# Performance work log

Measured on AMD Instinct MI355X. Metric: run time of the kernel, lower is better.

Reference implementation:

```python
import jax, jax.numpy as jnp
import numpy as np

HEADS = 4
DIM_HEAD = 32
SCALE = DIM_HEAD ** -0.5


def setup_inputs() -> dict:
    key = jax.random.key(0)
    k1, k2, k3 = jax.random.split(key, 3)
    dim = 128
    hidden = HEADS * DIM_HEAD  # 128
    x = jax.random.normal(k1, (4, dim, 64, 64), dtype=jnp.float32)
    w_qkv = jax.random.normal(k2, (3 * hidden, dim), dtype=jnp.float32) * (dim ** -0.5)
    w_out = jax.random.normal(k3, (dim, hidden), dtype=jnp.float32) * (hidden ** -0.5)
    b_out = jnp.zeros((dim,), dtype=jnp.float32)
    return {"x": x, "w_qkv": w_qkv, "w_out": w_out, "b_out": b_out}


def reference(x, w_qkv, w_out, b_out):
    b, c, h, w = x.shape
    n = h * w
    # 1x1 conv == channel matmul per pixel
    qkv = jnp.einsum('oc,bchw->bohw', w_qkv, x)  # [b, 3*hidden, h, w]
    q, k, v = jnp.split(qkv, 3, axis=1)
    # b (heads d) x y -> b heads d (x y)
    def to_heads(t):
        return t.reshape(b, HEADS, DIM_HEAD, n)
    q = to_heads(q) * SCALE
    k = to_heads(k)
    v = to_heads(v)
    sim = jnp.einsum('bhdi,bhdj->bhij', q, k)          # [b, heads, n, n]
    attn = jax.nn.softmax(sim, axis=-1)
    out = jnp.einsum('bhij,bhdj->bhid', attn, v)        # [b, heads, n, d]
    # b h (x y) d -> b (h d) x y
    out = out.transpose(0, 1, 3, 2).reshape(b, HEADS * DIM_HEAD, h, w)
    out = jnp.einsum('oc,bchw->bohw', w_out, out) + b_out[None, :, None, None]
    return out
```

## Files before the change

### kernel.cpp

```cpp
#include <hip/hip_runtime.h>
#include <math.h>

#define NHEAD 4
#define DHEAD 32
#define NPIX  4096
#define CIN   128

typedef __bf16 bf16_t;
typedef __bf16 bf16x8 __attribute__((ext_vector_type(8)));
typedef __bf16 bf16x4 __attribute__((ext_vector_type(4)));
typedef float  f32x4  __attribute__((ext_vector_type(4)));

constexpr float QSCALE = 0.17677669529663687f * 1.4426950408889634f;

__global__ void __launch_bounds__(256) prep_weights(
    const float* __restrict__ w_qkv, const float* __restrict__ w_out,
    ushort* __restrict__ wqkv_bf, ushort* __restrict__ wout_bf) {
  const int i4 = (blockIdx.x * 256 + threadIdx.x) * 4;
  const float* src;
  ushort* dst;
  float sc = 1.f;
  if (i4 < 49152) {
    src = w_qkv + i4; dst = wqkv_bf + i4;
    if (i4 < 16384) sc = QSCALE;
  } else {
    src = w_out + (i4 - 49152); dst = wout_bf + (i4 - 49152);
  }
  float4 v = *(const float4*)src;
  bf16x4 o = {(bf16_t)(v.x * sc), (bf16_t)(v.y * sc),
              (bf16_t)(v.z * sc), (bf16_t)(v.w * sc)};
  *(bf16x4*)dst = o;
}

__global__ void __launch_bounds__(384) qkv_mfma(
    const float* __restrict__ x, const ushort* __restrict__ wqkv,
    ushort* __restrict__ qb, ushort* __restrict__ kb, ushort* __restrict__ vT) {
  __shared__ ushort Xls[32 * 136];
  const int tid = threadIdx.x, cg = tid >> 6, lane = tid & 63;
  const int n = lane & 15, quad = lane >> 4;
  const int b = blockIdx.y, p0 = blockIdx.x * 32;

  bf16x8 wf[4][4];
#pragma unroll
  for (int t1 = 0; t1 < 4; ++t1)
#pragma unroll
    for (int k = 0; k < 4; ++k)
      wf[t1][k] = *(const bf16x8*)(wqkv +
          (size_t)(cg * 64 + t1 * 16 + n) * CIN + k * 32 + quad * 8);

  if (tid < 256) {
    const int pc = tid & 7;
    const int c  = (tid >> 3) * 4;
    const float* xp = x + ((size_t)b * CIN + c) * NPIX + p0 + pc * 4;
    float4 r0 = *(const float4*)xp;
    float4 r1 = *(const float4*)(xp + NPIX);
    float4 r2 = *(const float4*)(xp + 2 * NPIX);
    float4 r3 = *(const float4*)(xp + 3 * NPIX);
    bf16x4 w0 = {(bf16_t)r0.x, (bf16_t)r1.x, (bf16_t)r2.x, (bf16_t)r3.x};
    bf16x4 w1 = {(bf16_t)r0.y, (bf16_t)r1.y, (bf16_t)r2.y, (bf16_t)r3.y};
    bf16x4 w2 = {(bf16_t)r0.z, (bf16_t)r1.z, (bf16_t)r2.z, (bf16_t)r3.z};
    bf16x4 w3 = {(bf16_t)r0.w, (bf16_t)r1.w, (bf16_t)r2.w, (bf16_t)r3.w};
    *(bf16x4*)&Xls[(pc * 4 + 0) * 136 + c] = w0;
    *(bf16x4*)&Xls[(pc * 4 + 1) * 136 + c] = w1;
    *(bf16x4*)&Xls[(pc * 4 + 2) * 136 + c] = w2;
    *(bf16x4*)&Xls[(pc * 4 + 3) * 136 + c] = w3;
  }
  __syncthreads();

  f32x4 acc[4][2];
#pragma unroll
  for (int i = 0; i < 4; ++i)
#pragma unroll
    for (int j = 0; j < 2; ++j) acc[i][j] = (f32x4){0.f, 0.f, 0.f, 0.f};

  const bool isv = (cg >= 4);
#pragma unroll
  for (int k = 0; k < 4; ++k) {
    bf16x8 xf[2];
#pragma unroll
    for (int pt = 0; pt < 2; ++pt)
      xf[pt] = *(const bf16x8*)&Xls[(pt * 16 + n) * 136 + k * 32 + quad * 8];
    if (!isv) {
#pragma unroll
      for (int wt = 0; wt < 4; ++wt)
#pragma unroll
        for (int pt = 0; pt < 2; ++pt)
          acc[wt][pt] = __builtin_amdgcn_mfma_f32_16x16x32_bf16(
              wf[wt][k], xf[pt], acc[wt][pt], 0, 0, 0);
    } else {
#pragma unroll
      for (int ct = 0; ct < 4; ++ct)
#pragma unroll
        for (int pt = 0; pt < 2; ++pt)
          acc[ct][pt] = __builtin_amdgcn_mfma_f32_16x16x32_bf16(
              xf[pt], wf[ct][k], acc[ct][pt], 0, 0, 0);
    }
  }

  if (!isv) {
    ushort* dst0 = (cg < 2) ? qb : kb;
#pragma unroll
    for (int wt = 0; wt < 4; ++wt) {
      const int ch = (cg & 1) * 64 + wt * 16 + quad * 4;
      const int head = ch >> 5, d = ch & 31;
#pragma unroll
      for (int pt = 0; pt < 2; ++pt) {
        const int p = p0 + pt * 16 + n;
        f32x4 a = acc[wt][pt];
        bf16x4 o = {(bf16_t)a[0], (bf16_t)a[1], (bf16_t)a[2], (bf16_t)a[3]};
        *(bf16x4*)(dst0 + ((size_t)(b * NHEAD + head) * NPIX + p) * DHEAD + d) = o;
      }
    }
  } else {
#pragma unroll
    for (int ct = 0; ct < 4; ++ct) {
      const int ch = (cg & 1) * 64 + ct * 16 + n;
      const int head = ch >> 5, d = ch & 31;
#pragma unroll
      for (int pt = 0; pt < 2; ++pt) {
        const int p = p0 + pt * 16 + quad * 4;
        f32x4 a = acc[ct][pt];
        bf16x4 o = {(bf16_t)a[0], (bf16_t)a[1], (bf16_t)a[2], (bf16_t)a[3]};
        *(bf16x4*)(vT + ((size_t)(b * NHEAD + head) * DHEAD + d) * NPIX + p) = o;
      }
    }
  }
}

__device__ __forceinline__ void ft_load(const ushort* kb0, const ushort* vb0,
                                        int t, bf16x8* kf, bf16x8* vf) {
#pragma unroll
  for (int p = 0; p < 2; ++p) {
#pragma unroll
    for (int s = 0; s < 2; ++s)
      kf[p * 2 + s] = *(const bf16x8*)(kb0 + (size_t)(t * 64 + p * 32 + s * 4) * DHEAD);
#pragma unroll
    for (int dp = 0; dp < 2; ++dp)
      vf[p * 2 + dp] = *(const bf16x8*)(vb0 + (size_t)dp * 16 * NPIX + t * 64 + p * 32);
  }
}

__device__ __forceinline__ void ft_compute(const bf16x8* qf, const bf16x8* kf,
                                           const bf16x8* vf, const bf16x8 ones,
                                           f32x4 O[8][2], f32x4* Ol) {
  const f32x4 zero = {0.f, 0.f, 0.f, 0.f};
#pragma unroll
  for (int p = 0; p < 2; ++p) {
#pragma unroll
    for (int rp = 0; rp < 8; ++rp) {
      f32x4 sa = __builtin_amdgcn_mfma_f32_16x16x32_bf16(kf[p * 2 + 0], qf[rp], zero, 0, 0, 0);
      f32x4 sb = __builtin_amdgcn_mfma_f32_16x16x32_bf16(kf[p * 2 + 1], qf[rp], zero, 0, 0, 0);
      bf16x8 pf;
#pragma unroll
      for (int r = 0; r < 4; ++r) {
        pf[r]     = (bf16_t)__builtin_amdgcn_exp2f(sa[r]);
        pf[r + 4] = (bf16_t)__builtin_amdgcn_exp2f(sb[r]);
      }
      O[rp][0] = __builtin_amdgcn_mfma_f32_16x16x32_bf16(pf, vf[p * 2 + 0], O[rp][0], 0, 0, 0);
      O[rp][1] = __builtin_amdgcn_mfma_f32_16x16x32_bf16(pf, vf[p * 2 + 1], O[rp][1], 0, 0, 0);
      Ol[rp]   = __builtin_amdgcn_mfma_f32_16x16x32_bf16(pf, ones, Ol[rp], 0, 0, 0);
    }
  }
}

__global__ void __launch_bounds__(256, 2) flash_mfma(
    const ushort* __restrict__ qb, const ushort* __restrict__ kbuf,
    const ushort* __restrict__ vTb, float* __restrict__ part) {
  const int tid = threadIdx.x, wave = tid >> 6, lane = tid & 63;
  const int n = lane & 15, quad = lane >> 4;
  const int js = blockIdx.y, bh = blockIdx.z;
  const int qrel = blockIdx.x * 512 + wave * 128;

  const ushort* kg = kbuf + (size_t)bh * NPIX * DHEAD;
  const ushort* vg = vTb + (size_t)bh * DHEAD * NPIX;

  bf16x8 qf[8];
#pragma unroll
  for (int rp = 0; rp < 8; ++rp)
    qf[rp] = *(const bf16x8*)(qb +
        ((size_t)bh * NPIX + qrel + rp * 16 + n) * DHEAD + quad * 8);

  f32x4 O[8][2], Ol[8];
#pragma unroll
  for (int rp = 0; rp < 8; ++rp) {
    O[rp][0] = (f32x4){0.f, 0.f, 0.f, 0.f};
    O[rp][1] = (f32x4){0.f, 0.f, 0.f, 0.f};
    Ol[rp]   = (f32x4){0.f, 0.f, 0.f, 0.f};
  }
  const bf16_t one = (bf16_t)1.0f;
  const bf16x8 ones = {one, one, one, one, one, one, one, one};

  const int pk = ((n >> 2) << 3) | (n & 3);
  const ushort* kb0 = kg + (size_t)(js * 1024 + pk) * DHEAD + quad * 8;
  const ushort* vb0 = vg + (size_t)n * NPIX + js * 1024 + quad * 8;

  bf16x8 kA[4], vA[4], kB[4], vB[4];
  ft_load(kb0, vb0, 0, kA, vA);
#pragma unroll 1
  for (int t = 0; t < 16; t += 2) {
    ft_load(kb0, vb0, t + 1, kB, vB);
    ft_compute(qf, kA, vA, ones, O, Ol);
    if (t + 2 < 16) ft_load(kb0, vb0, t + 2, kA, vA);
    ft_compute(qf, kB, vB, ones, O, Ol);
  }

  float* pb = part + ((size_t)js * 65536 + (size_t)bh * NPIX + qrel) * 36;
#pragma unroll
  for (int rp = 0; rp < 8; ++rp)
#pragma unroll
    for (int r = 0; r < 4; ++r) {
      const int q = rp * 16 + quad * 4 + r;
      pb[(size_t)q * 36 + n]      = O[rp][0][r];
      pb[(size_t)q * 36 + 16 + n] = O[rp][1][r];
      if (n == 0) pb[(size_t)q * 36 + 32] = Ol[rp][r];
    }
}

__global__ void __launch_bounds__(256) combine4(
    const float* __restrict__ part, ushort* __restrict__ aoT) {
  const int idx = blockIdx.x * 256 + threadIdx.x;
  const float* p0 = part + (size_t)idx * 36;
  const float* p1 = p0 + (size_t)65536 * 36;
  const float* p2 = p1 + (size_t)65536 * 36;
  const float* p3 = p2 + (size_t)65536 * 36;
  const float inv = 1.f / (p0[32] + p1[32] + p2[32] + p3[32]);
#pragma unroll
  for (int t = 0; t < 4; ++t) {
    float4 a0 = ((const float4*)p0)[2 * t], a1 = ((const float4*)p0)[2 * t + 1];
    float4 b0 = ((const float4*)p1)[2 * t], b1 = ((const float4*)p1)[2 * t + 1];
    float4 c0 = ((const float4*)p2)[2 * t], c1 = ((const float4*)p2)[2 * t + 1];
    float4 d0 = ((const float4*)p3)[2 * t], d1 = ((const float4*)p3)[2 * t + 1];
    bf16x8 o = {(bf16_t)((a0.x + b0.x + c0.x + d0.x) * inv),
                (bf16_t)((a0.y + b0.y + c0.y + d0.y) * inv),
                (bf16_t)((a0.z + b0.z + c0.z + d0.z) * inv),
                (bf16_t)((a0.w + b0.w + c0.w + d0.w) * inv),
                (bf16_t)((a1.x + b1.x + c1.x + d1.x) * inv),
                (bf16_t)((a1.y + b1.y + c1.y + d1.y) * inv),
                (bf16_t)((a1.z + b1.z + c1.z + d1.z) * inv),
                (bf16_t)((a1.w + b1.w + c1.w + d1.w) * inv)};
    *(bf16x8*)(aoT + (size_t)idx * 32 + t * 8) = o;
  }
}

__global__ void __launch_bounds__(512) out_mfma(
    const ushort* __restrict__ aoT, const ushort* __restrict__ wob,
    const float* __restrict__ bias, float* __restrict__ out) {
  const int tid = threadIdx.x, wv = tid >> 6, lane = tid & 63;
  const int n = lane & 15, quad = lane >> 4;
  const int b = blockIdx.y;
  const int oc0 = (wv & 1) * 64;
  const int p = blockIdx.x * 64 + (wv >> 1) * 16 + n;

  bf16x8 wf[4][4];
#pragma unroll
  for (int mt = 0; mt < 4; ++mt)
#pragma unroll
    for (int k = 0; k < 4; ++k)
      wf[mt][k] = *(const bf16x8*)(wob + (size_t)(oc0 + mt * 16 + n) * CIN + k * 32 + quad * 8);

  bf16x8 bfr[4];
#pragma unroll
  for (int k = 0; k < 4; ++k)
    bfr[k] = *(const bf16x8*)(aoT + ((size_t)(b * NHEAD + k) * NPIX + p) * DHEAD + quad * 8);

  f32x4 acc[4];
#pragma unroll
  for (int mt = 0; mt < 4; ++mt) acc[mt] = (f32x4){0.f, 0.f, 0.f, 0.f};
#pragma unroll
  for (int k = 0; k < 4; ++k)
#pragma unroll
    for (int mt = 0; mt < 4; ++mt)
      acc[mt] = __builtin_amdgcn_mfma_f32_16x16x32_bf16(wf[mt][k], bfr[k], acc[mt], 0, 0, 0);

#pragma unroll
  for (int mt = 0; mt < 4; ++mt) {
    const int oc = oc0 + mt * 16 + quad * 4;
#pragma unroll
    for (int r = 0; r < 4; ++r)
      out[((size_t)b * CIN + oc + r) * NPIX + p] = acc[mt][r] + bias[oc + r];
  }
}

extern "C" void kernel_launch(void* const* d_in, const int* in_sizes, int n_in,
                              void* d_out, int out_size, void* d_ws, size_t ws_size,
                              hipStream_t stream) {
  const float* x     = (const float*)d_in[0];
  const float* w_qkv = (const float*)d_in[1];
  const float* w_out = (const float*)d_in[2];
  const float* b_out = (const float*)d_in[3];
  float* out = (float*)d_out;

  char* base = (char*)d_ws;
  ushort* qb      = (ushort*)base;
  ushort* kb      = (ushort*)(base + (size_t)4 * 1024 * 1024);
  ushort* vT      = (ushort*)(base + (size_t)8 * 1024 * 1024);
  ushort* aoT     = (ushort*)(base + (size_t)12 * 1024 * 1024);
  ushort* wqkv_bf = (ushort*)(base + (size_t)16 * 1024 * 1024);
  ushort* wout_bf = (ushort*)(base + (size_t)16 * 1024 * 1024 + 96 * 1024);
  float*  part    = (float*)(base + (size_t)17 * 1024 * 1024);

  prep_weights<<<dim3(64), 256, 0, stream>>>(w_qkv, w_out, wqkv_bf, wout_bf);
  qkv_mfma<<<dim3(128, 4), 384, 0, stream>>>(x, wqkv_bf, qb, kb, vT);
  flash_mfma<<<dim3(8, 4, 16), 256, 0, stream>>>(qb, kb, vT, part);
  combine4<<<dim3(256), 256, 0, stream>>>(part, aoT);
  out_mfma<<<dim3(64, 4), 512, 0, stream>>>(aoT, wout_bf, b_out, out);
}
```

Baseline: 140.4 us.

## Fuse split-KV combine into flash kernel and fold weight casts into GEMMs

The flash kernel now splits the keys across the four waves of a block instead of across grid blocks. Each wave holds 64 query rows and processes a 1024-key slice, and the partial sums are reduced through shared memory inside the kernel, so the separate combine kernel and its global partial buffer go away. The weight prep kernel is removed; the QKV and output GEMM kernels read fp32 weights and convert them (with the Q scale) in registers. This cuts two launches and a large global round trip, but each wave now does a smaller tile with less Q reuse, and the weights are converted redundantly in every block.

```diff
diff --git a/kernel.cpp b/kernel.cpp
--- a/kernel.cpp
+++ b/kernel.cpp
@@ -13,40 +13,28 @@
 
 constexpr float QSCALE = 0.17677669529663687f * 1.4426950408889634f;
 
-__global__ void __launch_bounds__(256) prep_weights(
-    const float* __restrict__ w_qkv, const float* __restrict__ w_out,
-    ushort* __restrict__ wqkv_bf, ushort* __restrict__ wout_bf) {
-  const int i4 = (blockIdx.x * 256 + threadIdx.x) * 4;
-  const float* src;
-  ushort* dst;
-  float sc = 1.f;
-  if (i4 < 49152) {
-    src = w_qkv + i4; dst = wqkv_bf + i4;
-    if (i4 < 16384) sc = QSCALE;
-  } else {
-    src = w_out + (i4 - 49152); dst = wout_bf + (i4 - 49152);
-  }
-  float4 v = *(const float4*)src;
-  bf16x4 o = {(bf16_t)(v.x * sc), (bf16_t)(v.y * sc),
-              (bf16_t)(v.z * sc), (bf16_t)(v.w * sc)};
-  *(bf16x4*)dst = o;
-}
-
 __global__ void __launch_bounds__(384) qkv_mfma(
-    const float* __restrict__ x, const ushort* __restrict__ wqkv,
+    const float* __restrict__ x, const float* __restrict__ wqkv,
     ushort* __restrict__ qb, ushort* __restrict__ kb, ushort* __restrict__ vT) {
   __shared__ ushort Xls[32 * 136];
   const int tid = threadIdx.x, cg = tid >> 6, lane = tid & 63;
   const int n = lane & 15, quad = lane >> 4;
   const int b = blockIdx.y, p0 = blockIdx.x * 32;
 
+  const float wsc = (cg < 2) ? QSCALE : 1.0f;
   bf16x8 wf[4][4];
 #pragma unroll
   for (int t1 = 0; t1 < 4; ++t1)
 #pragma unroll
-    for (int k = 0; k < 4; ++k)
-      wf[t1][k] = *(const bf16x8*)(wqkv +
-          (size_t)(cg * 64 + t1 * 16 + n) * CIN + k * 32 + quad * 8);
+    for (int k = 0; k < 4; ++k) {
+      const float* wp = wqkv + (size_t)(cg * 64 + t1 * 16 + n) * CIN + k * 32 + quad * 8;
+      float4 a = *(const float4*)wp;
+      float4 c = *(const float4*)(wp + 4);
+      wf[t1][k] = (bf16x8){(bf16_t)(a.x * wsc), (bf16_t)(a.y * wsc),
+                           (bf16_t)(a.z * wsc), (bf16_t)(a.w * wsc),
+                           (bf16_t)(c.x * wsc), (bf16_t)(c.y * wsc),
+                           (bf16_t)(c.z * wsc), (bf16_t)(c.w * wsc)};
+    }
 
   if (tid < 256) {
     const int pc = tid & 7;
@@ -127,62 +115,55 @@
   }
 }
 
-__device__ __forceinline__ void ft_load(const ushort* kb0, const ushort* vb0,
-                                        int t, bf16x8* kf, bf16x8* vf) {
-#pragma unroll
-  for (int p = 0; p < 2; ++p) {
-#pragma unroll
-    for (int s = 0; s < 2; ++s)
-      kf[p * 2 + s] = *(const bf16x8*)(kb0 + (size_t)(t * 64 + p * 32 + s * 4) * DHEAD);
-#pragma unroll
-    for (int dp = 0; dp < 2; ++dp)
-      vf[p * 2 + dp] = *(const bf16x8*)(vb0 + (size_t)dp * 16 * NPIX + t * 64 + p * 32);
-  }
-}
-
-__device__ __forceinline__ void ft_compute(const bf16x8* qf, const bf16x8* kf,
-                                           const bf16x8* vf, const bf16x8 ones,
-                                           f32x4 O[8][2], f32x4* Ol) {
+__device__ __forceinline__ void fl_load(const ushort* kb0, const ushort* vb0,
+                                        int st, bf16x8* f) {
+  f[0] = *(const bf16x8*)(kb0 + (size_t)(st * 32) * DHEAD);
+  f[1] = *(const bf16x8*)(kb0 + (size_t)(st * 32 + 4) * DHEAD);
+  f[2] = *(const bf16x8*)(vb0 + st * 32);
+  f[3] = *(const bf16x8*)(vb0 + (size_t)16 * NPIX + st * 32);
+}
+
+__device__ __forceinline__ void fl_compute(const bf16x8* qf, const bf16x8* f,
+                                           const bf16x8 ones,
+                                           f32x4 O[4][2], f32x4* Ol) {
   const f32x4 zero = {0.f, 0.f, 0.f, 0.f};
 #pragma unroll
-  for (int p = 0; p < 2; ++p) {
-#pragma unroll
-    for (int rp = 0; rp < 8; ++rp) {
-      f32x4 sa = __builtin_amdgcn_mfma_f32_16x16x32_bf16(kf[p * 2 + 0], qf[rp], zero, 0, 0, 0);
-      f32x4 sb = __builtin_amdgcn_mfma_f32_16x16x32_bf16(kf[p * 2 + 1], qf[rp], zero, 0, 0, 0);
-      bf16x8 pf;
-#pragma unroll
-      for (int r = 0; r < 4; ++r) {
-        pf[r]     = (bf16_t)__builtin_amdgcn_exp2f(sa[r]);
-        pf[r + 4] = (bf16_t)__builtin_amdgcn_exp2f(sb[r]);
-      }
-      O[rp][0] = __builtin_amdgcn_mfma_f32_16x16x32_bf16(pf, vf[p * 2 + 0], O[rp][0], 0, 0, 0);
-      O[rp][1] = __builtin_amdgcn_mfma_f32_16x16x32_bf16(pf, vf[p * 2 + 1], O[rp][1], 0, 0, 0);
-      Ol[rp]   = __builtin_amdgcn_mfma_f32_16x16x32_bf16(pf, ones, Ol[rp], 0, 0, 0);
-    }
-  }
-}
-
-__global__ void __launch_bounds__(256, 2) flash_mfma(
+  for (int rp = 0; rp < 4; ++rp) {
+    f32x4 sa = __builtin_amdgcn_mfma_f32_16x16x32_bf16(f[0], qf[rp], zero, 0, 0, 0);
+    f32x4 sb = __builtin_amdgcn_mfma_f32_16x16x32_bf16(f[1], qf[rp], zero, 0, 0, 0);
+    bf16x8 pf;
+#pragma unroll
+    for (int r = 0; r < 4; ++r) {
+      pf[r]     = (bf16_t)__builtin_amdgcn_exp2f(sa[r]);
+      pf[r + 4] = (bf16_t)__builtin_amdgcn_exp2f(sb[r]);
+    }
+    O[rp][0] = __builtin_amdgcn_mfma_f32_16x16x32_bf16(pf, f[2], O[rp][0], 0, 0, 0);
+    O[rp][1] = __builtin_amdgcn_mfma_f32_16x16x32_bf16(pf, f[3], O[rp][1], 0, 0, 0);
+    Ol[rp]   = __builtin_amdgcn_mfma_f32_16x16x32_bf16(pf, ones, Ol[rp], 0, 0, 0);
+  }
+}
+
+__global__ void __launch_bounds__(256, 4) flash_mfma(
     const ushort* __restrict__ qb, const ushort* __restrict__ kbuf,
-    const ushort* __restrict__ vTb, float* __restrict__ part) {
+    const ushort* __restrict__ vTb, ushort* __restrict__ aoT) {
+  __shared__ float Ols[4][64][34];
   const int tid = threadIdx.x, wave = tid >> 6, lane = tid & 63;
   const int n = lane & 15, quad = lane >> 4;
-  const int js = blockIdx.y, bh = blockIdx.z;
-  const int qrel = blockIdx.x * 512 + wave * 128;
+  const int bh = blockIdx.y;
+  const int q0 = blockIdx.x * 64;
 
   const ushort* kg = kbuf + (size_t)bh * NPIX * DHEAD;
   const ushort* vg = vTb + (size_t)bh * DHEAD * NPIX;
 
-  bf16x8 qf[8];
-#pragma unroll
-  for (int rp = 0; rp < 8; ++rp)
+  bf16x8 qf[4];
+#pragma unroll
+  for (int rp = 0; rp < 4; ++rp)
     qf[rp] = *(const bf16x8*)(qb +
-        ((size_t)bh * NPIX + qrel + rp * 16 + n) * DHEAD + quad * 8);
-
-  f32x4 O[8][2], Ol[8];
-#pragma unroll
-  for (int rp = 0; rp < 8; ++rp) {
+        ((size_t)bh * NPIX + q0 + rp * 16 + n) * DHEAD + quad * 8);
+
+  f32x4 O[4][2], Ol[4];
+#pragma unroll
+  for (int rp = 0; rp < 4; ++rp) {
     O[rp][0] = (f32x4){0.f, 0.f, 0.f, 0.f};
     O[rp][1] = (f32x4){0.f, 0.f, 0.f, 0.f};
     Ol[rp]   = (f32x4){0.f, 0.f, 0.f, 0.f};
@@ -191,59 +172,46 @@
   const bf16x8 ones = {one, one, one, one, one, one, one, one};
 
   const int pk = ((n >> 2) << 3) | (n & 3);
-  const ushort* kb0 = kg + (size_t)(js * 1024 + pk) * DHEAD + quad * 8;
-  const ushort* vb0 = vg + (size_t)n * NPIX + js * 1024 + quad * 8;
-
-  bf16x8 kA[4], vA[4], kB[4], vB[4];
-  ft_load(kb0, vb0, 0, kA, vA);
+  const ushort* kb0 = kg + (size_t)(wave * 1024 + pk) * DHEAD + quad * 8;
+  const ushort* vb0 = vg + (size_t)n * NPIX + wave * 1024 + quad * 8;
+
+  bf16x8 fA[4], fB[4];
+  fl_load(kb0, vb0, 0, fA);
 #pragma unroll 1
-  for (int t = 0; t < 16; t += 2) {
-    ft_load(kb0, vb0, t + 1, kB, vB);
-    ft_compute(qf, kA, vA, ones, O, Ol);
-    if (t + 2 < 16) ft_load(kb0, vb0, t + 2, kA, vA);
-    ft_compute(qf, kB, vB, ones, O, Ol);
-  }
-
-  float* pb = part + ((size_t)js * 65536 + (size_t)bh * NPIX + qrel) * 36;
-#pragma unroll
-  for (int rp = 0; rp < 8; ++rp)
+  for (int st = 0; st < 32; st += 2) {
+    fl_load(kb0, vb0, st + 1, fB);
+    fl_compute(qf, fA, ones, O, Ol);
+    if (st + 2 < 32) fl_load(kb0, vb0, st + 2, fA);
+    fl_compute(qf, fB, ones, O, Ol);
+  }
+
+  float* W = &Ols[wave][0][0];
+#pragma unroll
+  for (int rp = 0; rp < 4; ++rp)
 #pragma unroll
     for (int r = 0; r < 4; ++r) {
       const int q = rp * 16 + quad * 4 + r;
-      pb[(size_t)q * 36 + n]      = O[rp][0][r];
-      pb[(size_t)q * 36 + 16 + n] = O[rp][1][r];
-      if (n == 0) pb[(size_t)q * 36 + 32] = Ol[rp][r];
-    }
-}
-
-__global__ void __launch_bounds__(256) combine4(
-    const float* __restrict__ part, ushort* __restrict__ aoT) {
-  const int idx = blockIdx.x * 256 + threadIdx.x;
-  const float* p0 = part + (size_t)idx * 36;
-  const float* p1 = p0 + (size_t)65536 * 36;
-  const float* p2 = p1 + (size_t)65536 * 36;
-  const float* p3 = p2 + (size_t)65536 * 36;
-  const float inv = 1.f / (p0[32] + p1[32] + p2[32] + p3[32]);
-#pragma unroll
-  for (int t = 0; t < 4; ++t) {
-    float4 a0 = ((const float4*)p0)[2 * t], a1 = ((const float4*)p0)[2 * t + 1];
-    float4 b0 = ((const float4*)p1)[2 * t], b1 = ((const float4*)p1)[2 * t + 1];
-    float4 c0 = ((const float4*)p2)[2 * t], c1 = ((const float4*)p2)[2 * t + 1];
-    float4 d0 = ((const float4*)p3)[2 * t], d1 = ((const float4*)p3)[2 * t + 1];
-    bf16x8 o = {(bf16_t)((a0.x + b0.x + c0.x + d0.x) * inv),
-                (bf16_t)((a0.y + b0.y + c0.y + d0.y) * inv),
-                (bf16_t)((a0.z + b0.z + c0.z + d0.z) * inv),
-                (bf16_t)((a0.w + b0.w + c0.w + d0.w) * inv),
-                (bf16_t)((a1.x + b1.x + c1.x + d1.x) * inv),
-                (bf16_t)((a1.y + b1.y + c1.y + d1.y) * inv),
-                (bf16_t)((a1.z + b1.z + c1.z + d1.z) * inv),
-                (bf16_t)((a1.w + b1.w + c1.w + d1.w) * inv)};
-    *(bf16x8*)(aoT + (size_t)idx * 32 + t * 8) = o;
-  }
+      W[q * 34 + n]      = O[rp][0][r];
+      W[q * 34 + 16 + n] = O[rp][1][r];
+      if (n == 0) W[q * 34 + 32] = Ol[rp][r];
+    }
+  __syncthreads();
+
+  const int q = tid >> 2, dg = tid & 3;
+  const float l = Ols[0][q][32] + Ols[1][q][32] + Ols[2][q][32] + Ols[3][q][32];
+  const float inv = 1.f / l;
+  bf16x8 o8;
+#pragma unroll
+  for (int e = 0; e < 8; ++e) {
+    const int d = dg * 8 + e;
+    const float s = Ols[0][q][d] + Ols[1][q][d] + Ols[2][q][d] + Ols[3][q][d];
+    o8[e] = (bf16_t)(s * inv);
+  }
+  *(bf16x8*)(aoT + ((size_t)bh * NPIX + q0 + q) * DHEAD + dg * 8) = o8;
 }
 
 __global__ void __launch_bounds__(512) out_mfma(
-    const ushort* __restrict__ aoT, const ushort* __restrict__ wob,
+    const ushort* __restrict__ aoT, const float* __restrict__ wout,
     const float* __restrict__ bias, float* __restrict__ out) {
   const int tid = threadIdx.x, wv = tid >> 6, lane = tid & 63;
   const int n = lane & 15, quad = lane >> 4;
@@ -255,8 +223,13 @@
 #pragma unroll
   for (int mt = 0; mt < 4; ++mt)
 #pragma unroll
-    for (int k = 0; k < 4; ++k)
-      wf[mt][k] = *(const bf16x8*)(wob + (size_t)(oc0 + mt * 16 + n) * CIN + k * 32 + quad * 8);
+    for (int k = 0; k < 4; ++k) {
+      const float* wp = wout + (size_t)(oc0 + mt * 16 + n) * CIN + k * 32 + quad * 8;
+      float4 a = *(const float4*)wp;
+      float4 c = *(const float4*)(wp + 4);
+      wf[mt][k] = (bf16x8){(bf16_t)a.x, (bf16_t)a.y, (bf16_t)a.z, (bf16_t)a.w,
+                           (bf16_t)c.x, (bf16_t)c.y, (bf16_t)c.z, (bf16_t)c.w};
+    }
 
   bf16x8 bfr[4];
 #pragma unroll
@@ -291,17 +264,12 @@
   float* out = (float*)d_out;
 
   char* base = (char*)d_ws;
-  ushort* qb      = (ushort*)base;
-  ushort* kb      = (ushort*)(base + (size_t)4 * 1024 * 1024);
-  ushort* vT      = (ushort*)(base + (size_t)8 * 1024 * 1024);
-  ushort* aoT     = (ushort*)(base + (size_t)12 * 1024 * 1024);
-  ushort* wqkv_bf = (ushort*)(base + (size_t)16 * 1024 * 1024);
-  ushort* wout_bf = (ushort*)(base + (size_t)16 * 1024 * 1024 + 96 * 1024);
-  float*  part    = (float*)(base + (size_t)17 * 1024 * 1024);
-
-  prep_weights<<<dim3(64), 256, 0, stream>>>(w_qkv, w_out, wqkv_bf, wout_bf);
-  qkv_mfma<<<dim3(128, 4), 384, 0, stream>>>(x, wqkv_bf, qb, kb, vT);
-  flash_mfma<<<dim3(8, 4, 16), 256, 0, stream>>>(qb, kb, vT, part);
-  combine4<<<dim3(256), 256, 0, stream>>>(part, aoT);
-  out_mfma<<<dim3(64, 4), 512, 0, stream>>>(aoT, wout_bf, b_out, out);
-}
+  ushort* qb  = (ushort*)base;
+  ushort* kb  = (ushort*)(base + (size_t)4 * 1024 * 1024);
+  ushort* vT  = (ushort*)(base + (size_t)8 * 1024 * 1024);
+  ushort* aoT = (ushort*)(base + (size_t)12 * 1024 * 1024);
+
+  qkv_mfma<<<dim3(128, 4), 384, 0, stream>>>(x, w_qkv, qb, kb, vT);
+  flash_mfma<<<dim3(64, 16), 256, 0, stream>>>(qb, kb, vT, aoT);
+  out_mfma<<<dim3(64, 4), 512, 0, stream>>>(aoT, w_out, b_out, out);
+}
```

Result: faster. 136.1 us (-3.1%).
